# Kernel optimization log

Hardware: AMD Instinct MI355X
Metric: run time of the kernel (lower is better)

The kernel has to match this reference:

```python
import jax, jax.numpy as jnp
import numpy as np


def bitnet_quantize(w):
    # scale = mean(|w|) clamped; ternary round of centered/scaled weights; STE
    scale = jnp.maximum(jnp.mean(jnp.abs(w)), 1e-8)
    w_centered = w - jnp.mean(w)
    w_bin = jnp.round(jnp.clip(w_centered / scale, -1.0, 1.0))
    w_q = jax.lax.stop_gradient(w_bin - w) + w  # forward: w_bin, grad: identity
    return w_q, scale


def setup_inputs() -> dict:
    key = jax.random.key(0)
    kx, kr, ki, kj, kk = jax.random.split(key, 5)
    B, S, F = 4, 4096, 2048
    C = F // 4  # 512 quaternion channels
    init_std = 0.02
    return {
        "x": jax.random.normal(kx, (B, S, F), dtype=jnp.float32),
        "r_weight": jax.random.normal(kr, (C, C), dtype=jnp.float32) * init_std,
        "i_weight": jax.random.normal(ki, (C, C), dtype=jnp.float32) * init_std,
        "j_weight": jax.random.normal(kj, (C, C), dtype=jnp.float32) * init_std,
        "k_weight": jax.random.normal(kk, (C, C), dtype=jnp.float32) * init_std,
        "bias": jnp.zeros((F,), dtype=jnp.float32),
    }


def reference(x, r_weight, i_weight, j_weight, k_weight, bias):
    # eval path of QuatBitLinear: ternary-quantize all 4 weights, shared scale
    r_w, s1 = bitnet_quantize(r_weight)
    i_w, s2 = bitnet_quantize(i_weight)
    j_w, s3 = bitnet_quantize(j_weight)
    k_w, s4 = bitnet_quantize(k_weight)
    scale = (s1 + s2 + s3 + s4) / 4.0

    r_in, i_in, j_in, k_in = jnp.split(x, 4, axis=-1)  # each [B,S,C]

    def lin(v, w):  # F.linear: v @ w.T
        return jnp.einsum('bsc,oc->bso', v, w)

    r_out = lin(r_in, r_w) - lin(i_in, i_w) - lin(j_in, j_w) - lin(k_in, k_w)
    i_out = lin(r_in, i_w) + lin(i_in, r_w) + lin(j_in, k_w) - lin(k_in, j_w)
    j_out = lin(r_in, j_w) - lin(i_in, k_w) + lin(j_in, r_w) + lin(k_in, i_w)
    k_out = lin(r_in, k_w) + lin(i_in, j_w) - lin(j_in, i_w) + lin(k_in, r_w)

    out = jnp.concatenate([r_out, i_out, j_out, k_out], axis=-1)
    out = out + bias  # bias added BEFORE scaling, as in the torch code
    return out * scale * 0.5
```

## Files before the change

### kernel.cpp

```cpp
#include <hip/hip_runtime.h>
#include <hip/hip_bf16.h>
#include <stdint.h>

typedef __attribute__((ext_vector_type(8))) short short8;
typedef __attribute__((ext_vector_type(4))) float f32x4;
typedef __attribute__((ext_vector_type(4))) float float4v;
typedef __attribute__((ext_vector_type(4))) unsigned short ushort4v;

static constexpr int C = 512;
static constexpr int F = 2048;
static constexpr int NW = C * C;

__device__ inline unsigned short f2bf(float f) {
    union { float f; unsigned int u; } cv;
    cv.f = f;
    unsigned int r = cv.u + 0x7fffu + ((cv.u >> 16) & 1u);
    return (unsigned short)(r >> 16);
}

__global__ void qb_prep(const float* __restrict__ X, unsigned short* __restrict__ Xb, int n8,
                        const float* __restrict__ w0, const float* __restrict__ w1,
                        const float* __restrict__ w2, const float* __restrict__ w3,
                        double* __restrict__ part) {
    __shared__ double red[8];
    if (blockIdx.x >= 2048) {
        int b = blockIdx.x - 2048;
        int wid = b >> 6, chunk = b & 63;
        const float* wsel = (wid == 0) ? w0 : (wid == 1) ? w1 : (wid == 2) ? w2 : w3;
        const float* p = wsel + chunk * (NW / 64);
        double sa = 0.0, sv = 0.0;
        for (int i = threadIdx.x; i < (NW / 64) / 4; i += 256) {
            float4v v = ((const float4v*)p)[i];
            sa += (double)fabsf(v.x) + fabsf(v.y) + fabsf(v.z) + fabsf(v.w);
            sv += (double)v.x + v.y + v.z + v.w;
        }
        for (int off = 32; off; off >>= 1) {
            sa += __shfl_down(sa, off);
            sv += __shfl_down(sv, off);
        }
        int wv = threadIdx.x >> 6;
        if ((threadIdx.x & 63) == 0) { red[wv] = sa; red[4 + wv] = sv; }
        __syncthreads();
        if (threadIdx.x == 0) {
            part[b * 2 + 0] = red[0] + red[1] + red[2] + red[3];
            part[b * 2 + 1] = red[4] + red[5] + red[6] + red[7];
        }
        return;
    }
    int stride = 2048 * 256;
    for (int i = blockIdx.x * 256 + threadIdx.x; i < n8; i += stride) {
        float4v a = ((const float4v*)X)[2 * i];
        float4v b = ((const float4v*)X)[2 * i + 1];
        short8 h;
        h[0] = (short)f2bf(a[0]); h[1] = (short)f2bf(a[1]);
        h[2] = (short)f2bf(a[2]); h[3] = (short)f2bf(a[3]);
        h[4] = (short)f2bf(b[0]); h[5] = (short)f2bf(b[1]);
        h[6] = (short)f2bf(b[2]); h[7] = (short)f2bf(b[3]);
        ((short8*)Xb)[i] = h;
    }
}

__global__ void qb_build(const float* __restrict__ w0, const float* __restrict__ w1,
                         const float* __restrict__ w2, const float* __restrict__ w3,
                         const double* __restrict__ part, unsigned short* __restrict__ Wb,
                         double* __restrict__ finals) {
    int wid = blockIdx.x >> 7;
    int t = (blockIdx.x & 127) * 256 + threadIdx.x;
    int o = t >> 6;
    int c0 = (t & 63) << 3;
    double sa = 0.0, sv = 0.0;
#pragma unroll
    for (int i = 0; i < 64; ++i) {
        sa += part[(wid * 64 + i) * 2 + 0];
        sv += part[(wid * 64 + i) * 2 + 1];
    }
    float mf = (float)(sv * (1.0 / NW));
    float scf = fmaxf((float)(sa * (1.0 / NW)), 1e-8f);
    if ((blockIdx.x & 127) == 0 && threadIdx.x == 0) finals[wid] = (double)scf;

    const float sgn[4][4] = {{ 1.f, 1.f, 1.f, 1.f},
                             {-1.f, 1.f, 1.f,-1.f},
                             {-1.f,-1.f, 1.f, 1.f},
                             {-1.f, 1.f,-1.f, 1.f}};
    const float* wptr[4] = {w0, w1, w2, w3};
    const float* w = wptr[wid] + o * C + c0;
    float4v va = ((const float4v*)w)[0];
    float4v vb = ((const float4v*)w)[1];
    float q[8];
#pragma unroll
    for (int e = 0; e < 4; ++e) {
        q[e]     = rintf(fminf(fmaxf((va[e] - mf) / scf, -1.f), 1.f));
        q[4 + e] = rintf(fminf(fmaxf((vb[e] - mf) / scf, -1.f), 1.f));
    }
#pragma unroll
    for (int p = 0; p < 4; ++p) {
        int qb = p ^ wid;
        float s = sgn[wid][p];
        short8 v;
#pragma unroll
        for (int e = 0; e < 8; ++e) v[e] = (short)f2bf(s * q[e]);
        *(short8*)&Wb[(size_t)(p * C + o) * F + qb * C + c0] = v;
    }
}

__global__ __launch_bounds__(512, 2) void qb_gemm256(
    const unsigned short* __restrict__ A,
    const unsigned short* __restrict__ B,
    const float* __restrict__ bias, const double* __restrict__ finals,
    float* __restrict__ out) {
    constexpr int K = F, N = F, BK = 64, NT = K / BK;
    __shared__ unsigned short As[2][256 * 64];
    __shared__ unsigned short Bs[2][256 * 64];

    const int tid = threadIdx.x;
    const int lane = tid & 63;
    const int w = tid >> 6;
    const int wm = w >> 2, wn = w & 3;

    const int nbn = N / 256;
    const int nwg = gridDim.x;
    const int bid = blockIdx.x;
    const int swz = (bid & 7) * (nwg >> 3) + (bid >> 3);
    const int bm = swz / nbn, bn = swz % nbn;
    const int brow = bm * 256, bcol = bn * 256;

    const int frow = lane & 15;
    const int fk = (lane >> 4) << 3;

    auto stage = [&](const unsigned short* __restrict__ gbase, int growbase,
                     unsigned short* ldsbase, int h, int kt) {
        int ktw = kt & (NT - 1);
#pragma unroll
        for (int l = 0; l < 2; ++l) {
            int boff = h * 16384 + (w * 2 + l) * 1024 + lane * 16;
            int e = boff >> 1;
            int r = e >> 6, c = e & 63;
            int csrc = c ^ ((r & 7) << 3);
            const unsigned short* src = gbase + (size_t)(growbase + r) * K + ktw * BK + csrc;
            __builtin_amdgcn_global_load_lds(
                (const __attribute__((address_space(1))) void*)src,
                (__attribute__((address_space(3))) void*)((char*)ldsbase + boff),
                16, 0, 0);
        }
    };
    auto rdA = [&](int buf, int mh, int ks, int mi) -> short8 {
        int r = mh * 128 + wm * 64 + mi * 16 + frow;
        int cs = (ks * 32 + fk) ^ ((r & 7) << 3);
        return *(const short8*)&As[buf][r * 64 + cs];
    };
    auto rdB = [&](int buf, int nh, int ks, int ni) -> short8 {
        int r = nh * 128 + wn * 32 + ni * 16 + frow;
        int cs = (ks * 32 + fk) ^ ((r & 7) << 3);
        return *(const short8*)&Bs[buf][r * 64 + cs];
    };

    f32x4 acc[2][4][2][2];
#pragma unroll
    for (int a0 = 0; a0 < 2; ++a0)
#pragma unroll
        for (int a1 = 0; a1 < 4; ++a1)
#pragma unroll
            for (int a2 = 0; a2 < 2; ++a2)
#pragma unroll
                for (int a3 = 0; a3 < 2; ++a3) acc[a0][a1][a2][a3] = (f32x4){0.f, 0.f, 0.f, 0.f};

    stage(B, bcol, &Bs[0][0], 0, 0);
    stage(A, brow, &As[0][0], 0, 0);
    stage(A, brow, &As[0][0], 1, 0);
    stage(B, bcol, &Bs[0][0], 1, 0);
    stage(B, bcol, &Bs[1][0], 0, 1);
    stage(A, brow, &As[1][0], 0, 1);
    asm volatile("s_waitcnt vmcnt(4)" ::: "memory");
    __builtin_amdgcn_s_barrier();

    short8 af[2][4], b0[2][2], b1[2][2];
#pragma unroll
    for (int ks = 0; ks < 2; ++ks)
#pragma unroll
        for (int ni = 0; ni < 2; ++ni) b0[ks][ni] = rdB(0, 0, ks, ni);

#define QB_MFMA(MH, NH, BB)                                                            \
    _Pragma("unroll") for (int ks = 0; ks < 2; ++ks)                                   \
        _Pragma("unroll") for (int mi = 0; mi < 4; ++mi)                               \
            _Pragma("unroll") for (int ni = 0; ni < 2; ++ni)                           \
                acc[MH][mi][NH][ni] = __builtin_amdgcn_mfma_f32_16x16x32_bf16(         \
                    af[ks][mi], BB[ks][ni], acc[MH][mi][NH][ni], 0, 0, 0);

#define QB_TILE(CB, KT)                                                                \
                                           \
    _Pragma("unroll") for (int ks = 0; ks < 2; ++ks)                                   \
        _Pragma("unroll") for (int mi = 0; mi < 4; ++mi) af[ks][mi] = rdA(CB, 0, ks, mi); \
    stage(A, brow, &As[1 - (CB)][0], 1, (KT) + 1);                                     \
    __builtin_amdgcn_s_barrier();                                                      \
    asm volatile("s_waitcnt lgkmcnt(0)" ::: "memory");                                 \
    __builtin_amdgcn_sched_barrier(0);                                                 \
    __builtin_amdgcn_s_setprio(1);                                                     \
    QB_MFMA(0, 0, b0)                                                                  \
    __builtin_amdgcn_s_setprio(0);                                                     \
    __builtin_amdgcn_s_barrier();                                                      \
                                             \
    _Pragma("unroll") for (int ks = 0; ks < 2; ++ks)                                   \
        _Pragma("unroll") for (int ni = 0; ni < 2; ++ni) b1[ks][ni] = rdB(CB, 1, ks, ni); \
    stage(B, bcol, &Bs[1 - (CB)][0], 1, (KT) + 1);                                     \
    __builtin_amdgcn_s_barrier();                                                      \
    asm volatile("s_waitcnt lgkmcnt(0)" ::: "memory");                                 \
    __builtin_amdgcn_sched_barrier(0);                                                 \
    __builtin_amdgcn_s_setprio(1);                                                     \
    QB_MFMA(0, 1, b1)                                                                  \
    __builtin_amdgcn_s_setprio(0);                                                     \
    __builtin_amdgcn_s_barrier();                                                      \
                                             \
    _Pragma("unroll") for (int ks = 0; ks < 2; ++ks)                                   \
        _Pragma("unroll") for (int mi = 0; mi < 4; ++mi) af[ks][mi] = rdA(CB, 1, ks, mi); \
    stage(B, bcol, &Bs[CB][0], 0, (KT) + 2);                                           \
    __builtin_amdgcn_s_barrier();                                                      \
    asm volatile("s_waitcnt lgkmcnt(0)" ::: "memory");                                 \
    __builtin_amdgcn_sched_barrier(0);                                                 \
    __builtin_amdgcn_s_setprio(1);                                                     \
    QB_MFMA(1, 1, b1)                                                                  \
    __builtin_amdgcn_s_setprio(0);                                                     \
    __builtin_amdgcn_s_barrier();                                                      \
          \
    stage(A, brow, &As[CB][0], 0, (KT) + 2);                                           \
    __builtin_amdgcn_s_barrier();                                                      \
    __builtin_amdgcn_s_setprio(1);                                                     \
    QB_MFMA(1, 0, b0)                                                                  \
    __builtin_amdgcn_s_setprio(0);                                                     \
    asm volatile("s_waitcnt vmcnt(4)" ::: "memory");                                   \
    _Pragma("unroll") for (int ks = 0; ks < 2; ++ks)                                   \
        _Pragma("unroll") for (int ni = 0; ni < 2; ++ni) b0[ks][ni] = rdB(1 - (CB), 0, ks, ni); \
    __builtin_amdgcn_s_barrier();

    for (int it = 0; it < NT / 2; ++it) {
        int kt0 = 2 * it;
        QB_TILE(0, kt0)
        QB_TILE(1, kt0 + 1)
    }
#undef QB_TILE
#undef QB_MFMA

    float mul = (float)((finals[0] + finals[1] + finals[2] + finals[3]) * (0.25 * 0.5));

#pragma unroll
    for (int mh = 0; mh < 2; ++mh)
#pragma unroll
        for (int nh = 0; nh < 2; ++nh)
#pragma unroll
            for (int ni = 0; ni < 2; ++ni) {
                int gcol = bcol + nh * 128 + wn * 32 + ni * 16 + frow;
                float bv = bias[gcol];
#pragma unroll
                for (int mi = 0; mi < 4; ++mi) {
                    int gr0 = brow + mh * 128 + wm * 64 + mi * 16 + ((lane >> 4) << 2);
#pragma unroll
                    for (int j = 0; j < 4; ++j)
                        out[(size_t)(gr0 + j) * N + gcol] = (acc[mh][mi][nh][ni][j] + bv) * mul;
                }
            }
}

__global__ __launch_bounds__(256) void qb_gemm(
    const float* __restrict__ X, const unsigned short* __restrict__ Wb,
    const float* __restrict__ bias, const double* __restrict__ finals,
    float* __restrict__ out, int M) {
    constexpr int Kd = F, Nd = F;
    __shared__ unsigned short As[128 * 32];
    __shared__ unsigned short Bs[128 * 32];
    const int t = threadIdx.x;
    const int lane = t & 63, wv = t >> 6;
    const int nbn = Nd / 128;
    const int nwg = gridDim.x;
    const int bid = blockIdx.x;
    const int swz = (bid & 7) * (nwg >> 3) + (bid >> 3);
    const int bm = swz / nbn, bn = swz % nbn;
    const int brow = bm * 128, bcol = bn * 128;
    const int wr = wv >> 1, wc = wv & 1;
    const int frow = lane & 15;
    const int k8 = (lane >> 4) << 3;
    f32x4 acc[4][4];
#pragma unroll
    for (int i = 0; i < 4; ++i)
#pragma unroll
        for (int j = 0; j < 4; ++j) acc[i][j] = (f32x4){0.f, 0.f, 0.f, 0.f};
    const int ar = t >> 3;
    const int ac = (t & 7) << 2;
    for (int kk = 0; kk < Kd; kk += 32) {
#pragma unroll
        for (int is = 0; is < 2; ++is) {
            int idx = is * 2048 + t * 8;
            int row = idx >> 5, col = idx & 31;
            const unsigned short* src = &Wb[(size_t)(bcol + row) * Kd + kk + col];
            __builtin_amdgcn_global_load_lds(
                (const __attribute__((address_space(1))) void*)src,
                (__attribute__((address_space(3))) void*)&Bs[idx], 16, 0, 0);
        }
#pragma unroll
        for (int it = 0; it < 4; ++it) {
            int row = it * 32 + ar;
            float4v v = *(const float4v*)&X[(size_t)(brow + row) * Kd + kk + ac];
            ushort4v h;
            h[0] = f2bf(v[0]); h[1] = f2bf(v[1]); h[2] = f2bf(v[2]); h[3] = f2bf(v[3]);
            *(ushort4v*)&As[row * 32 + ac] = h;
        }
        __syncthreads();
        short8 a[4], b[4];
#pragma unroll
        for (int mi = 0; mi < 4; ++mi)
            a[mi] = *(const short8*)&As[(wr * 64 + mi * 16 + frow) * 32 + k8];
#pragma unroll
        for (int ni = 0; ni < 4; ++ni)
            b[ni] = *(const short8*)&Bs[(wc * 64 + ni * 16 + frow) * 32 + k8];
#pragma unroll
        for (int mi = 0; mi < 4; ++mi)
#pragma unroll
            for (int ni = 0; ni < 4; ++ni)
                acc[mi][ni] = __builtin_amdgcn_mfma_f32_16x16x32_bf16(
                    a[mi], b[ni], acc[mi][ni], 0, 0, 0);
        __syncthreads();
    }
    float mul = (float)((finals[0] + finals[1] + finals[2] + finals[3]) * (0.25 * 0.5));
#pragma unroll
    for (int ni = 0; ni < 4; ++ni) {
        int gcol = bcol + wc * 64 + ni * 16 + frow;
        float bv = bias[gcol];
#pragma unroll
        for (int mi = 0; mi < 4; ++mi) {
            int growb = brow + wr * 64 + mi * 16 + ((lane >> 4) << 2);
#pragma unroll
            for (int j = 0; j < 4; ++j)
                out[(size_t)(growb + j) * Nd + gcol] = (acc[mi][ni][j] + bv) * mul;
        }
    }
}

extern "C" void kernel_launch(void* const* d_in, const int* in_sizes, int n_in,
                              void* d_out, int out_size, void* d_ws, size_t ws_size,
                              hipStream_t stream) {
    const float* x    = (const float*)d_in[0];
    const float* wr_  = (const float*)d_in[1];
    const float* wi_  = (const float*)d_in[2];
    const float* wj_  = (const float*)d_in[3];
    const float* wk_  = (const float*)d_in[4];
    const float* bias = (const float*)d_in[5];
    float* out = (float*)d_out;
    const int M = in_sizes[0] / F;

    const size_t FIN_OFF = 4096;
    const size_t WB_OFF  = 8192;
    const size_t XB_OFF  = WB_OFF + (size_t)F * F * 2;
    const size_t NEED    = XB_OFF + (size_t)M * F * 2;

    double* part   = (double*)d_ws;
    double* finals = (double*)((char*)d_ws + FIN_OFF);
    unsigned short* Wb = (unsigned short*)((char*)d_ws + WB_OFF);
    unsigned short* Xb = (unsigned short*)((char*)d_ws + XB_OFF);

    const bool fast = (ws_size >= NEED) && (M % 256) == 0;

    qb_prep<<<2304, 256, 0, stream>>>(x, Xb, fast ? (M * F) / 8 : 0,
                                      wr_, wi_, wj_, wk_, part);
    qb_build<<<512, 256, 0, stream>>>(wr_, wi_, wj_, wk_, part, Wb, finals);

    if (fast) {
        const int grid = (M / 256) * (F / 256);
        qb_gemm256<<<grid, 512, 0, stream>>>(Xb, Wb, bias, finals, out);
    } else {
        const int grid = (M / 128) * (F / 128);
        qb_gemm<<<grid, 256, 0, stream>>>(x, Wb, bias, finals, out, M);
    }
}
```

Baseline: 387.6 us.

## Replace interleaved quarter-tile pipeline with simple double-buffered full-tile loop

Replaces the hand-scheduled four-phase K-tile loop, which interleaved LDS fragment reads, partial global-to-LDS stages and MFMA groups behind many barriers, with a plain double-buffered loop. Each iteration reads every A and B fragment for the current buffer, issues all loads for tile t+2 into that same buffer, and then runs all 64 MFMAs. Global source pointers are precomputed outside the loop to cut per-stage address arithmetic. The aim is fewer barriers and simpler scheduling, at the cost of more live fragment registers and less overlap between LDS reads and MFMA work.

```diff
diff --git a/kernel.cpp b/kernel.cpp
--- a/kernel.cpp
+++ b/kernel.cpp
@@ -127,21 +127,37 @@
     const int frow = lane & 15;
     const int fk = (lane >> 4) << 3;
 
-    auto stage = [&](const unsigned short* __restrict__ gbase, int growbase,
-                     unsigned short* ldsbase, int h, int kt) {
-        int ktw = kt & (NT - 1);
+    int boff[2][2];
+    const unsigned short* gpA[2][2];
+    const unsigned short* gpB[2][2];
+#pragma unroll
+    for (int h = 0; h < 2; ++h)
 #pragma unroll
         for (int l = 0; l < 2; ++l) {
-            int boff = h * 16384 + (w * 2 + l) * 1024 + lane * 16;
-            int e = boff >> 1;
+            int bo = h * 16384 + (w * 2 + l) * 1024 + lane * 16;
+            int e = bo >> 1;
             int r = e >> 6, c = e & 63;
             int csrc = c ^ ((r & 7) << 3);
-            const unsigned short* src = gbase + (size_t)(growbase + r) * K + ktw * BK + csrc;
-            __builtin_amdgcn_global_load_lds(
-                (const __attribute__((address_space(1))) void*)src,
-                (__attribute__((address_space(3))) void*)((char*)ldsbase + boff),
-                16, 0, 0);
-        }
+            boff[h][l] = bo;
+            gpA[h][l] = A + (size_t)(brow + r) * K + csrc;
+            gpB[h][l] = B + (size_t)(bcol + r) * K + csrc;
+        }
+
+    auto stageAll = [&](int bufI, int kt) {
+        int ko = (kt & (NT - 1)) * BK;
+        char* la = (char*)&As[bufI][0];
+        char* lb = (char*)&Bs[bufI][0];
+#pragma unroll
+        for (int h = 0; h < 2; ++h)
+#pragma unroll
+            for (int l = 0; l < 2; ++l) {
+                __builtin_amdgcn_global_load_lds(
+                    (const __attribute__((address_space(1))) void*)(gpA[h][l] + ko),
+                    (__attribute__((address_space(3))) void*)(la + boff[h][l]), 16, 0, 0);
+                __builtin_amdgcn_global_load_lds(
+                    (const __attribute__((address_space(1))) void*)(gpB[h][l] + ko),
+                    (__attribute__((address_space(3))) void*)(lb + boff[h][l]), 16, 0, 0);
+            }
     };
     auto rdA = [&](int buf, int mh, int ks, int mi) -> short8 {
         int r = mh * 128 + wm * 64 + mi * 16 + frow;
@@ -164,80 +180,48 @@
 #pragma unroll
                 for (int a3 = 0; a3 < 2; ++a3) acc[a0][a1][a2][a3] = (f32x4){0.f, 0.f, 0.f, 0.f};
 
-    stage(B, bcol, &Bs[0][0], 0, 0);
-    stage(A, brow, &As[0][0], 0, 0);
-    stage(A, brow, &As[0][0], 1, 0);
-    stage(B, bcol, &Bs[0][0], 1, 0);
-    stage(B, bcol, &Bs[1][0], 0, 1);
-    stage(A, brow, &As[1][0], 0, 1);
-    asm volatile("s_waitcnt vmcnt(4)" ::: "memory");
+    stageAll(0, 0);
+    stageAll(1, 1);
+    asm volatile("s_waitcnt vmcnt(8)" ::: "memory");
     __builtin_amdgcn_s_barrier();
 
-    short8 af[2][4], b0[2][2], b1[2][2];
-#pragma unroll
-    for (int ks = 0; ks < 2; ++ks)
-#pragma unroll
-        for (int ni = 0; ni < 2; ++ni) b0[ks][ni] = rdB(0, 0, ks, ni);
-
-#define QB_MFMA(MH, NH, BB)                                                            \
-    _Pragma("unroll") for (int ks = 0; ks < 2; ++ks)                                   \
-        _Pragma("unroll") for (int mi = 0; mi < 4; ++mi)                               \
-            _Pragma("unroll") for (int ni = 0; ni < 2; ++ni)                           \
-                acc[MH][mi][NH][ni] = __builtin_amdgcn_mfma_f32_16x16x32_bf16(         \
-                    af[ks][mi], BB[ks][ni], acc[MH][mi][NH][ni], 0, 0, 0);
-
-#define QB_TILE(CB, KT)                                                                \
-                                           \
-    _Pragma("unroll") for (int ks = 0; ks < 2; ++ks)                                   \
-        _Pragma("unroll") for (int mi = 0; mi < 4; ++mi) af[ks][mi] = rdA(CB, 0, ks, mi); \
-    stage(A, brow, &As[1 - (CB)][0], 1, (KT) + 1);                                     \
-    __builtin_amdgcn_s_barrier();                                                      \
-    asm volatile("s_waitcnt lgkmcnt(0)" ::: "memory");                                 \
-    __builtin_amdgcn_sched_barrier(0);                                                 \
-    __builtin_amdgcn_s_setprio(1);                                                     \
-    QB_MFMA(0, 0, b0)                                                                  \
-    __builtin_amdgcn_s_setprio(0);                                                     \
-    __builtin_amdgcn_s_barrier();                                                      \
-                                             \
-    _Pragma("unroll") for (int ks = 0; ks < 2; ++ks)                                   \
-        _Pragma("unroll") for (int ni = 0; ni < 2; ++ni) b1[ks][ni] = rdB(CB, 1, ks, ni); \
-    stage(B, bcol, &Bs[1 - (CB)][0], 1, (KT) + 1);                                     \
-    __builtin_amdgcn_s_barrier();                                                      \
-    asm volatile("s_waitcnt lgkmcnt(0)" ::: "memory");                                 \
-    __builtin_amdgcn_sched_barrier(0);                                                 \
-    __builtin_amdgcn_s_setprio(1);                                                     \
-    QB_MFMA(0, 1, b1)                                                                  \
-    __builtin_amdgcn_s_setprio(0);                                                     \
-    __builtin_amdgcn_s_barrier();                                                      \
-                                             \
-    _Pragma("unroll") for (int ks = 0; ks < 2; ++ks)                                   \
-        _Pragma("unroll") for (int mi = 0; mi < 4; ++mi) af[ks][mi] = rdA(CB, 1, ks, mi); \
-    stage(B, bcol, &Bs[CB][0], 0, (KT) + 2);                                           \
-    __builtin_amdgcn_s_barrier();                                                      \
-    asm volatile("s_waitcnt lgkmcnt(0)" ::: "memory");                                 \
-    __builtin_amdgcn_sched_barrier(0);                                                 \
-    __builtin_amdgcn_s_setprio(1);                                                     \
-    QB_MFMA(1, 1, b1)                                                                  \
-    __builtin_amdgcn_s_setprio(0);                                                     \
-    __builtin_amdgcn_s_barrier();                                                      \
-          \
-    stage(A, brow, &As[CB][0], 0, (KT) + 2);                                           \
-    __builtin_amdgcn_s_barrier();                                                      \
-    __builtin_amdgcn_s_setprio(1);                                                     \
-    QB_MFMA(1, 0, b0)                                                                  \
-    __builtin_amdgcn_s_setprio(0);                                                     \
-    asm volatile("s_waitcnt vmcnt(4)" ::: "memory");                                   \
-    _Pragma("unroll") for (int ks = 0; ks < 2; ++ks)                                   \
-        _Pragma("unroll") for (int ni = 0; ni < 2; ++ni) b0[ks][ni] = rdB(1 - (CB), 0, ks, ni); \
-    __builtin_amdgcn_s_barrier();
-
-    for (int it = 0; it < NT / 2; ++it) {
-        int kt0 = 2 * it;
-        QB_TILE(0, kt0)
-        QB_TILE(1, kt0 + 1)
-    }
-#undef QB_TILE
-#undef QB_MFMA
+    for (int t = 0; t < NT; ++t) {
+        const int buf = t & 1;
+        short8 a[2][4][2];
+        short8 b[2][2][2];
+#pragma unroll
+        for (int mh = 0; mh < 2; ++mh)
+#pragma unroll
+            for (int mi = 0; mi < 4; ++mi)
+#pragma unroll
+                for (int ks = 0; ks < 2; ++ks) a[mh][mi][ks] = rdA(buf, mh, ks, mi);
+#pragma unroll
+        for (int nh = 0; nh < 2; ++nh)
+#pragma unroll
+            for (int ni = 0; ni < 2; ++ni)
+#pragma unroll
+                for (int ks = 0; ks < 2; ++ks) b[nh][ni][ks] = rdB(buf, nh, ks, ni);
+        asm volatile("s_waitcnt lgkmcnt(0)" ::: "memory");
+        __builtin_amdgcn_sched_barrier(0);
+        __builtin_amdgcn_s_barrier();
+        stageAll(buf, t + 2);
+        __builtin_amdgcn_s_setprio(1);
+#pragma unroll
+        for (int mh = 0; mh < 2; ++mh)
+#pragma unroll
+            for (int mi = 0; mi < 4; ++mi)
+#pragma unroll
+                for (int nh = 0; nh < 2; ++nh)
+#pragma unroll
+                    for (int ni = 0; ni < 2; ++ni)
+#pragma unroll
+                        for (int ks = 0; ks < 2; ++ks)
+                            acc[mh][mi][nh][ni] = __builtin_amdgcn_mfma_f32_16x16x32_bf16(
+                                a[mh][mi][ks], b[nh][ni][ks], acc[mh][mi][nh][ni], 0, 0, 0);
+        __builtin_amdgcn_s_setprio(0);
+        asm volatile("s_waitcnt vmcnt(8)" ::: "memory");
+        __builtin_amdgcn_s_barrier();
+    }
 
     float mul = (float)((finals[0] + finals[1] + finals[2] + finals[3]) * (0.25 * 0.5));
 
```

Measured after the change: 365.0 us. 5.8% less time.
